# Optimization experiments

Hardware: AMD Instinct MI355X
Metric: run time of the kernel (lower is better)

Reference implementation:

```python
import jax, jax.numpy as jnp
from jax import lax
import numpy as np

N_BINS = 8
SIGMA = (1.0, 2.0)
ALPHA = (1.0, 2.0, 4.0)
BETA = (0.02, 0.05)
KSIZE = 7
BOUNDS = (0.0, 1.0)
C, H, W = 3, 512, 512


def gaussian_kernel(size, s):
    # matches torch: linspace(-size//2+1, size//2, size) == arange(size)-size//2 for odd size
    x = jnp.arange(size, dtype=jnp.float32) - size // 2
    g = jnp.exp(-(x[:, None] ** 2 + x[None, :] ** 2) / (2.0 * s ** 2))
    return g / jnp.sum(g)


def setup_inputs() -> dict:
    key = jax.random.key(0)
    im_th = jax.random.uniform(key, (H, W, C), dtype=jnp.float32)
    sks = max(3, int(SIGMA[-1] * 4))
    if sks % 2 == 0:
        sks += 1
    sigma_kernels = jnp.stack([gaussian_kernel(sks, s) for s in SIGMA])      # (S, Ks, Ks)
    alpha_kernels = jnp.stack([gaussian_kernel(KSIZE, a) for a in ALPHA])    # (A, k, k)
    edges = jnp.linspace(BOUNDS[0], BOUNDS[1], N_BINS + 1, dtype=jnp.float32)
    bin_centers = (edges[1:] + edges[:-1]) / 2.0                             # (N,)
    betas = jnp.array(BETA, dtype=jnp.float32)                               # (B,)
    return dict(im_th=im_th, sigma_kernels=sigma_kernels,
                alpha_kernels=alpha_kernels, bin_centers=bin_centers, betas=betas)


def _conv_per_channel(x, k):
    # x: (M, H, W); k: (K, kh, kw) -> (M, K, H, W). Channels treated as batch,
    # equivalent to torch grouped conv with groups=M and K kernels per group.
    p = k.shape[-1] // 2
    return lax.conv_general_dilated(x[:, None], k[:, None], (1, 1),
                                    [(p, p), (p, p)],
                                    dimension_numbers=('NCHW', 'OIHW', 'NCHW'))


def reference(im_th, sigma_kernels, alpha_kernels, bin_centers, betas):
    x = jnp.clip(im_th, 0.0, 1.0).transpose(2, 0, 1)  # (C, H, W)
    C_, H_, W_ = x.shape
    S = sigma_kernels.shape[0]
    A = alpha_kernels.shape[0]
    B = betas.shape[0]
    N = bin_centers.shape[0]
    # per-channel blur at each sigma: (C, S, H, W)
    conv = _conv_per_channel(x, sigma_kernels)
    # gaussian soft-binning: (B, N, C, S, H, W)
    diff = conv[None, None] - bin_centers[None, :, None, None, None, None]
    bv = betas[:, None, None, None, None, None]
    iso = jnp.exp(-0.5 * (diff / bv) ** 2) / (jnp.sqrt(2.0 * jnp.pi) * bv)
    # depthwise alpha aggregation over all B*N*C*S channels: (M, A, H, W)
    out = _conv_per_channel(iso.reshape(B * N * C_ * S, H_, W_), alpha_kernels)
    loi = out.reshape(B, N, C_, S, A, H_, W_).transpose(4, 0, 3, 2, 5, 6, 1)
    return loi  # (A, B, S, C, H, W, N)
```

## Files before the change

### kernel.cpp

```cpp
#include <hip/hip_runtime.h>
#include <hip/hip_fp16.h>

#define IMH 512
#define IMW 512


__device__ __forceinline__ __half2 bc_h2(int v) {
  union { int i; __half2 h; } u; u.i = v; return u.h;
}
__device__ __forceinline__ int bc_i(__half2 v) {
  union { int i; __half2 h; } u; u.h = v; return u.i;
}

__global__ __launch_bounds__(256, 6) void loi_fused(
    const float* __restrict__ im,
    const float* __restrict__ sigk,
    const float* __restrict__ alphak,
    const float* __restrict__ binc,
    const float* __restrict__ betas,
    float* __restrict__ out)
{
  const int t     = threadIdx.x;
  const int combo = blockIdx.z;
  const int b     = combo / 6;
  const int sc    = combo % 6;
  const int s     = sc / 3;
  const int c     = sc % 3;
  const int tx0   = blockIdx.x * 32;
  const int ty0   = blockIdx.y * 8;

  __shared__ __align__(16) float smt[560];
  __shared__ __align__(16) unsigned char uni[23104];
  __shared__ float kf[3][8];
  __shared__ float sf[12];

  float*  imt = (float*)uni;
  float*  svt = (float*)(uni + 4224);
  __half* iso = (__half*)uni;
  __half* vv  = (__half*)(uni + 8512);

  for (int e = t; e < 1056; e += 256) {
    int j = e / 48, i = e - j * 48;
    float v = 0.f;
    if (i < 46) {
      int gy = ty0 + j - 7, gx = tx0 + i - 7;
      if (gy >= 0 && gy < IMH && gx >= 0 && gx < IMW) {
        v = im[(gy * IMW + gx) * 3 + c];
        v = fminf(fmaxf(v, 0.f), 1.f);
      }
    }
    imt[e] = v;
  }
  if (t < 9) {
    float acc = 0.f;
    #pragma unroll
    for (int j = 0; j < 9; j++) acc += sigk[s * 81 + t * 9 + j];
    sf[t] = acc;
  }
  if (t >= 32 && t < 56) {
    int a = (t - 32) >> 3, d = t & 7;
    float v = 0.f;
    if (d < 7) {
      #pragma unroll
      for (int j = 0; j < 7; j++) v += alphak[a * 49 + d * 7 + j];
    }
    kf[a][d] = v;
  }
  __syncthreads();

  for (int e = t; e < 672; e += 256) {
    int rr = e / 48, i = e - rr * 48;
    if (i < 46) {
      float acc = 0.f;
      #pragma unroll
      for (int d = 0; d < 9; d++) acc = fmaf(sf[d], imt[(rr + d) * 48 + i], acc);
      svt[e] = acc;
    }
  }
  __syncthreads();

  for (int e = t; e < 560; e += 256) {
    int rr = e / 40, j = e - rr * 40;
    if (j < 38) {
      float acc = 0.f;
      #pragma unroll
      for (int d = 0; d < 9; d++) acc = fmaf(sf[d], svt[rr * 48 + j + d], acc);
      smt[e] = acc;
    }
  }
  __syncthreads();

  const float beta = betas[b];
  const float norm = 0.39894228040143268f / beta;
  const float c2   = -0.72134752044448170f / (beta * beta);
  const int   np   = t & 3;
  const float ctr0 = binc[2 * np];
  const float ctr1 = binc[2 * np + 1];
  for (int u = t; u < 2128; u += 256) {
    int q  = u >> 2;
    int rr = q / 38, jj = q - rr * 38;
    float v  = smt[rr * 40 + jj];
    float t0 = v - ctr0, t1 = v - ctr1;
    float E0 = exp2f(t0 * t0 * c2) * norm;
    float E1 = exp2f(t1 * t1 * c2) * norm;
    int X = tx0 + jj - 3, Y = ty0 + rr - 3;
    if (!(((unsigned)X < IMW) && ((unsigned)Y < IMH))) { E0 = 0.f; E1 = 0.f; }
    *(__half2*)(iso + q * 8 + np * 2) = __floats2half2_rn(E0, E1);
  }
  __syncthreads();

  __half2 kh[3][7];
  #pragma unroll
  for (int a = 0; a < 3; a++)
    #pragma unroll
    for (int d = 0; d < 7; d++) kh[a][d] = __float2half2_rn(kf[a][d]);

  for (int g = t; g < 304; g += 256) {
    int yr = g / 38, jj = g - yr * 38;
    const int base = yr * 38 + jj;
    __half2 acc[3][4];
    #pragma unroll
    for (int a = 0; a < 3; a++)
      #pragma unroll
      for (int q = 0; q < 4; q++) acc[a][q] = __floats2half2_rn(0.f, 0.f);
    #pragma unroll
    for (int d = 0; d < 7; d++) {
      int4 raw = *(const int4*)(iso + ((base + d * 38) << 3));
      __half2 w0 = bc_h2(raw.x), w1 = bc_h2(raw.y);
      __half2 w2 = bc_h2(raw.z), w3 = bc_h2(raw.w);
      #pragma unroll
      for (int a = 0; a < 3; a++) {
        acc[a][0] = __hfma2(kh[a][d], w0, acc[a][0]);
        acc[a][1] = __hfma2(kh[a][d], w1, acc[a][1]);
        acc[a][2] = __hfma2(kh[a][d], w2, acc[a][2]);
        acc[a][3] = __hfma2(kh[a][d], w3, acc[a][3]);
      }
    }
    #pragma unroll
    for (int a = 0; a < 3; a++) {
      int4 o;
      o.x = bc_i(acc[a][0]); o.y = bc_i(acc[a][1]);
      o.z = bc_i(acc[a][2]); o.w = bc_i(acc[a][3]);
      *(int4*)(vv + ((((a << 3) + yr) * 38 + jj) << 3)) = o;
    }
  }
  __syncthreads();

  const int col = t & 31;
  const int row = t >> 5;
  float* op = out + ((size_t)combo << 21)
                  + ((size_t)(ty0 + row) * 512 + (tx0 + col)) * 8;
  #pragma unroll
  for (int a = 0; a < 3; a++) {
    const int base = ((a << 3) + row) * 38 + col;
    __half2 pA0, pA1, pA2, pA3, pB0, pB1, pB2, pB3;
    {
      int4 r0 = *(const int4*)(vv + (base << 3));
      pA0 = __hmul2(kh[a][0], bc_h2(r0.x)); pA1 = __hmul2(kh[a][0], bc_h2(r0.y));
      pA2 = __hmul2(kh[a][0], bc_h2(r0.z)); pA3 = __hmul2(kh[a][0], bc_h2(r0.w));
      int4 r1 = *(const int4*)(vv + ((base + 1) << 3));
      pB0 = __hmul2(kh[a][1], bc_h2(r1.x)); pB1 = __hmul2(kh[a][1], bc_h2(r1.y));
      pB2 = __hmul2(kh[a][1], bc_h2(r1.z)); pB3 = __hmul2(kh[a][1], bc_h2(r1.w));
    }
    #pragma unroll
    for (int d = 2; d < 7; d += 2) {
      int4 rA = *(const int4*)(vv + ((base + d) << 3));
      pA0 = __hfma2(kh[a][d], bc_h2(rA.x), pA0);
      pA1 = __hfma2(kh[a][d], bc_h2(rA.y), pA1);
      pA2 = __hfma2(kh[a][d], bc_h2(rA.z), pA2);
      pA3 = __hfma2(kh[a][d], bc_h2(rA.w), pA3);
      if (d + 1 < 7) {
        int4 rB = *(const int4*)(vv + ((base + d + 1) << 3));
        pB0 = __hfma2(kh[a][d + 1], bc_h2(rB.x), pB0);
        pB1 = __hfma2(kh[a][d + 1], bc_h2(rB.y), pB1);
        pB2 = __hfma2(kh[a][d + 1], bc_h2(rB.z), pB2);
        pB3 = __hfma2(kh[a][d + 1], bc_h2(rB.w), pB3);
      }
    }
    float2 a0 = __half22float2(pA0), b0 = __half22float2(pB0);
    float2 a1 = __half22float2(pA1), b1 = __half22float2(pB1);
    float2 a2 = __half22float2(pA2), b2 = __half22float2(pB2);
    float2 a3 = __half22float2(pA3), b3 = __half22float2(pB3);
    float4 lo = make_float4(a0.x + b0.x, a0.y + b0.y, a1.x + b1.x, a1.y + b1.y);
    float4 hi = make_float4(a2.x + b2.x, a2.y + b2.y, a3.x + b3.x, a3.y + b3.y);
    float* p = op + ((size_t)(a * 12) << 21);
    *(float4*)p       = lo;
    *(float4*)(p + 4) = hi;
  }
}

extern "C" void kernel_launch(void* const* d_in, const int* in_sizes, int n_in,
                              void* d_out, int out_size, void* d_ws, size_t ws_size,
                              hipStream_t stream)
{
  const float* im   = (const float*)d_in[0];
  const float* sigk = (const float*)d_in[1];
  const float* alpk = (const float*)d_in[2];
  const float* binc = (const float*)d_in[3];
  const float* bets = (const float*)d_in[4];
  float* out = (float*)d_out;

  loi_fused<<<dim3(16, 64, 12), 256, 0, stream>>>(im, sigk, alpk, binc, bets, out);
}
```

Baseline: 324.8 us.

## Enlarge tile to 32x16 and fuse separable alpha pass into register accumulation

Doubles the output tile height to 16 rows, which shrinks halo overhead per output pixel. The two-pass half-precision alpha convolution is replaced by a single pass: each thread does the horizontal pass in fp16 and scatters results into fp32 register accumulators for four output rows. This removes the intermediate shared buffer and one barrier, and folds the normalization into the kernel weights. The sigma blur passes are vectorized with float4, and each thread now computes all eight bins. The vertical pass now accumulates in fp32, which changes precision slightly, and the extra accumulators raise register pressure.

```diff
diff --git a/kernel.cpp b/kernel.cpp
--- a/kernel.cpp
+++ b/kernel.cpp
@@ -3,6 +3,8 @@
 
 #define IMH 512
 #define IMW 512
+#define TW  32
+#define TH  16
 
 
 __device__ __forceinline__ __half2 bc_h2(int v) {
@@ -12,7 +14,7 @@
   union { int i; __half2 h; } u; u.h = v; return u.i;
 }
 
-__global__ __launch_bounds__(256, 6) void loi_fused(
+__global__ __launch_bounds__(256, 8) void loi_fused(
     const float* __restrict__ im,
     const float* __restrict__ sigk,
     const float* __restrict__ alphak,
@@ -26,25 +28,24 @@
   const int sc    = combo % 6;
   const int s     = sc / 3;
   const int c     = sc % 3;
-  const int tx0   = blockIdx.x * 32;
-  const int ty0   = blockIdx.y * 8;
-
-  __shared__ __align__(16) float smt[560];
-  __shared__ __align__(16) unsigned char uni[23104];
+  const int tx0   = blockIdx.x * TW;
+  const int ty0   = blockIdx.y * TH;
+
+  __shared__ __align__(16) float smt[22 * 40];
+  __shared__ __align__(16) unsigned char uni[13376];
   __shared__ float kf[3][8];
   __shared__ float sf[12];
 
   float*  imt = (float*)uni;
-  float*  svt = (float*)(uni + 4224);
+  float*  svt = (float*)(uni + 5760);
   __half* iso = (__half*)uni;
-  __half* vv  = (__half*)(uni + 8512);
-
-  for (int e = t; e < 1056; e += 256) {
+
+  for (int e = t; e < 1440; e += 256) {
     int j = e / 48, i = e - j * 48;
     float v = 0.f;
     if (i < 46) {
       int gy = ty0 + j - 7, gx = tx0 + i - 7;
-      if (gy >= 0 && gy < IMH && gx >= 0 && gx < IMW) {
+      if ((unsigned)gy < IMH && (unsigned)gx < IMW) {
         v = im[(gy * IMW + gx) * 3 + c];
         v = fminf(fmaxf(v, 0.f), 1.f);
       }
@@ -68,124 +69,135 @@
   }
   __syncthreads();
 
-  for (int e = t; e < 672; e += 256) {
-    int rr = e / 48, i = e - rr * 48;
-    if (i < 46) {
-      float acc = 0.f;
-      #pragma unroll
-      for (int d = 0; d < 9; d++) acc = fmaf(sf[d], imt[(rr + d) * 48 + i], acc);
-      svt[e] = acc;
-    }
-  }
-  __syncthreads();
-
-  for (int e = t; e < 560; e += 256) {
-    int rr = e / 40, j = e - rr * 40;
-    if (j < 38) {
-      float acc = 0.f;
-      #pragma unroll
-      for (int d = 0; d < 9; d++) acc = fmaf(sf[d], svt[rr * 48 + j + d], acc);
-      smt[e] = acc;
-    }
+  for (int u = t; u < 264; u += 256) {
+    int rr = u / 12, cu = u - rr * 12;
+    const float* p = imt + rr * 48 + cu * 4;
+    float4 acc = make_float4(0.f, 0.f, 0.f, 0.f);
+    #pragma unroll
+    for (int d = 0; d < 9; d++) {
+      float4 w = *(const float4*)(p + d * 48);
+      float sd = sf[d];
+      acc.x = fmaf(sd, w.x, acc.x); acc.y = fmaf(sd, w.y, acc.y);
+      acc.z = fmaf(sd, w.z, acc.z); acc.w = fmaf(sd, w.w, acc.w);
+    }
+    *(float4*)(svt + rr * 48 + cu * 4) = acc;
+  }
+  __syncthreads();
+
+  for (int u = t; u < 220; u += 256) {
+    int rr = u / 10, cu = u - rr * 10;
+    const float* p = svt + rr * 48 + cu * 4;
+    float v[16];
+    #pragma unroll
+    for (int q = 0; q < 4; q++) {
+      float4 w = *(const float4*)(p + q * 4);
+      v[4 * q + 0] = w.x; v[4 * q + 1] = w.y;
+      v[4 * q + 2] = w.z; v[4 * q + 3] = w.w;
+    }
+    float o0 = 0.f, o1 = 0.f, o2 = 0.f, o3 = 0.f;
+    #pragma unroll
+    for (int d = 0; d < 9; d++) {
+      float sd = sf[d];
+      o0 = fmaf(sd, v[d + 0], o0); o1 = fmaf(sd, v[d + 1], o1);
+      o2 = fmaf(sd, v[d + 2], o2); o3 = fmaf(sd, v[d + 3], o3);
+    }
+    *(float4*)(smt + rr * 40 + cu * 4) = make_float4(o0, o1, o2, o3);
   }
   __syncthreads();
 
   const float beta = betas[b];
+  const float c2   = -0.72134752044448170f / (beta * beta);
+  float bc0 = binc[0], bc1 = binc[1], bc2 = binc[2], bc3 = binc[3];
+  float bc4 = binc[4], bc5 = binc[5], bc6 = binc[6], bc7 = binc[7];
+  for (int p = t; p < 836; p += 256) {
+    int rr = p / 38, jj = p - rr * 38;
+    float v = smt[rr * 40 + jj];
+    int X = tx0 + jj - 3, Y = ty0 + rr - 3;
+    float msk = (((unsigned)X < IMW) && ((unsigned)Y < IMH)) ? 1.f : 0.f;
+    float t0 = v - bc0, t1 = v - bc1, t2 = v - bc2, t3 = v - bc3;
+    float t4 = v - bc4, t5 = v - bc5, t6 = v - bc6, t7 = v - bc7;
+    float E0 = exp2f(t0 * t0 * c2) * msk, E1 = exp2f(t1 * t1 * c2) * msk;
+    float E2 = exp2f(t2 * t2 * c2) * msk, E3 = exp2f(t3 * t3 * c2) * msk;
+    float E4 = exp2f(t4 * t4 * c2) * msk, E5 = exp2f(t5 * t5 * c2) * msk;
+    float E6 = exp2f(t6 * t6 * c2) * msk, E7 = exp2f(t7 * t7 * c2) * msk;
+    int4 w;
+    w.x = bc_i(__floats2half2_rn(E0, E1));
+    w.y = bc_i(__floats2half2_rn(E2, E3));
+    w.z = bc_i(__floats2half2_rn(E4, E5));
+    w.w = bc_i(__floats2half2_rn(E6, E7));
+    *(int4*)(iso + p * 8) = w;
+  }
+  __syncthreads();
+
   const float norm = 0.39894228040143268f / beta;
-  const float c2   = -0.72134752044448170f / (beta * beta);
-  const int   np   = t & 3;
-  const float ctr0 = binc[2 * np];
-  const float ctr1 = binc[2 * np + 1];
-  for (int u = t; u < 2128; u += 256) {
-    int q  = u >> 2;
-    int rr = q / 38, jj = q - rr * 38;
-    float v  = smt[rr * 40 + jj];
-    float t0 = v - ctr0, t1 = v - ctr1;
-    float E0 = exp2f(t0 * t0 * c2) * norm;
-    float E1 = exp2f(t1 * t1 * c2) * norm;
-    int X = tx0 + jj - 3, Y = ty0 + rr - 3;
-    if (!(((unsigned)X < IMW) && ((unsigned)Y < IMH))) { E0 = 0.f; E1 = 0.f; }
-    *(__half2*)(iso + q * 8 + np * 2) = __floats2half2_rn(E0, E1);
-  }
-  __syncthreads();
-
   __half2 kh[3][7];
+  float   kvf[3][7];
   #pragma unroll
   for (int a = 0; a < 3; a++)
     #pragma unroll
-    for (int d = 0; d < 7; d++) kh[a][d] = __float2half2_rn(kf[a][d]);
-
-  for (int g = t; g < 304; g += 256) {
-    int yr = g / 38, jj = g - yr * 38;
-    const int base = yr * 38 + jj;
-    __half2 acc[3][4];
-    #pragma unroll
-    for (int a = 0; a < 3; a++)
-      #pragma unroll
-      for (int q = 0; q < 4; q++) acc[a][q] = __floats2half2_rn(0.f, 0.f);
-    #pragma unroll
     for (int d = 0; d < 7; d++) {
-      int4 raw = *(const int4*)(iso + ((base + d * 38) << 3));
-      __half2 w0 = bc_h2(raw.x), w1 = bc_h2(raw.y);
-      __half2 w2 = bc_h2(raw.z), w3 = bc_h2(raw.w);
+      float f = kf[a][d];
+      kh[a][d]  = __float2half2_rn(f);
+      kvf[a][d] = f * norm;
+    }
+
+  const int ng  = t & 1;
+  const int col = (t >> 1) & 31;
+  const int rq  = t >> 6;
+  const int r0  = rq * 4;
+
+  float4 acc[4][3];
+  #pragma unroll
+  for (int j = 0; j < 4; j++)
+    #pragma unroll
+    for (int a = 0; a < 3; a++) acc[j][a] = make_float4(0.f, 0.f, 0.f, 0.f);
+
+  const __half* ibase = iso + ((r0 * 38 + col) * 8 + ng * 4);
+  #pragma unroll
+  for (int m = 0; m < 10; m++) {
+    const __half* prow = ibase + m * 304;
+    __half2 h0[3], h1[3];
+    #pragma unroll
+    for (int a = 0; a < 3; a++) {
+      h0[a] = __float2half2_rn(0.f);
+      h1[a] = __float2half2_rn(0.f);
+    }
+    #pragma unroll
+    for (int e = 0; e < 7; e++) {
+      int2 ve = *(const int2*)(prow + e * 8);
+      __half2 lo = bc_h2(ve.x), hi = bc_h2(ve.y);
       #pragma unroll
       for (int a = 0; a < 3; a++) {
-        acc[a][0] = __hfma2(kh[a][d], w0, acc[a][0]);
-        acc[a][1] = __hfma2(kh[a][d], w1, acc[a][1]);
-        acc[a][2] = __hfma2(kh[a][d], w2, acc[a][2]);
-        acc[a][3] = __hfma2(kh[a][d], w3, acc[a][3]);
+        h0[a] = __hfma2(kh[a][e], lo, h0[a]);
+        h1[a] = __hfma2(kh[a][e], hi, h1[a]);
       }
     }
     #pragma unroll
     for (int a = 0; a < 3; a++) {
-      int4 o;
-      o.x = bc_i(acc[a][0]); o.y = bc_i(acc[a][1]);
-      o.z = bc_i(acc[a][2]); o.w = bc_i(acc[a][3]);
-      *(int4*)(vv + ((((a << 3) + yr) * 38 + jj) << 3)) = o;
-    }
-  }
-  __syncthreads();
-
-  const int col = t & 31;
-  const int row = t >> 5;
-  float* op = out + ((size_t)combo << 21)
-                  + ((size_t)(ty0 + row) * 512 + (tx0 + col)) * 8;
-  #pragma unroll
-  for (int a = 0; a < 3; a++) {
-    const int base = ((a << 3) + row) * 38 + col;
-    __half2 pA0, pA1, pA2, pA3, pB0, pB1, pB2, pB3;
-    {
-      int4 r0 = *(const int4*)(vv + (base << 3));
-      pA0 = __hmul2(kh[a][0], bc_h2(r0.x)); pA1 = __hmul2(kh[a][0], bc_h2(r0.y));
-      pA2 = __hmul2(kh[a][0], bc_h2(r0.z)); pA3 = __hmul2(kh[a][0], bc_h2(r0.w));
-      int4 r1 = *(const int4*)(vv + ((base + 1) << 3));
-      pB0 = __hmul2(kh[a][1], bc_h2(r1.x)); pB1 = __hmul2(kh[a][1], bc_h2(r1.y));
-      pB2 = __hmul2(kh[a][1], bc_h2(r1.z)); pB3 = __hmul2(kh[a][1], bc_h2(r1.w));
-    }
-    #pragma unroll
-    for (int d = 2; d < 7; d += 2) {
-      int4 rA = *(const int4*)(vv + ((base + d) << 3));
-      pA0 = __hfma2(kh[a][d], bc_h2(rA.x), pA0);
-      pA1 = __hfma2(kh[a][d], bc_h2(rA.y), pA1);
-      pA2 = __hfma2(kh[a][d], bc_h2(rA.z), pA2);
-      pA3 = __hfma2(kh[a][d], bc_h2(rA.w), pA3);
-      if (d + 1 < 7) {
-        int4 rB = *(const int4*)(vv + ((base + d + 1) << 3));
-        pB0 = __hfma2(kh[a][d + 1], bc_h2(rB.x), pB0);
-        pB1 = __hfma2(kh[a][d + 1], bc_h2(rB.y), pB1);
-        pB2 = __hfma2(kh[a][d + 1], bc_h2(rB.z), pB2);
-        pB3 = __hfma2(kh[a][d + 1], bc_h2(rB.w), pB3);
+      float2 f0 = __half22float2(h0[a]);
+      float2 f1 = __half22float2(h1[a]);
+      #pragma unroll
+      for (int j = 0; j < 4; j++) {
+        if (m - j >= 0 && m - j <= 6) {
+          float w = kvf[a][m - j];
+          acc[j][a].x = fmaf(w, f0.x, acc[j][a].x);
+          acc[j][a].y = fmaf(w, f0.y, acc[j][a].y);
+          acc[j][a].z = fmaf(w, f1.x, acc[j][a].z);
+          acc[j][a].w = fmaf(w, f1.y, acc[j][a].w);
+        }
       }
     }
-    float2 a0 = __half22float2(pA0), b0 = __half22float2(pB0);
-    float2 a1 = __half22float2(pA1), b1 = __half22float2(pB1);
-    float2 a2 = __half22float2(pA2), b2 = __half22float2(pB2);
-    float2 a3 = __half22float2(pA3), b3 = __half22float2(pB3);
-    float4 lo = make_float4(a0.x + b0.x, a0.y + b0.y, a1.x + b1.x, a1.y + b1.y);
-    float4 hi = make_float4(a2.x + b2.x, a2.y + b2.y, a3.x + b3.x, a3.y + b3.y);
-    float* p = op + ((size_t)(a * 12) << 21);
-    *(float4*)p       = lo;
-    *(float4*)(p + 4) = hi;
+  }
+
+  const int gx = tx0 + col;
+  #pragma unroll
+  for (int j = 0; j < 4; j++) {
+    const int gy = ty0 + r0 + j;
+    float* op = out + ((size_t)combo << 21)
+                    + ((size_t)gy * 512 + gx) * 8 + ng * 4;
+    *(float4*)op                          = acc[j][0];
+    *(float4*)(op + ((size_t)12 << 21))   = acc[j][1];
+    *(float4*)(op + ((size_t)24 << 21))   = acc[j][2];
   }
 }
 
@@ -200,5 +212,6 @@
   const float* bets = (const float*)d_in[4];
   float* out = (float*)d_out;
 
-  loi_fused<<<dim3(16, 64, 12), 256, 0, stream>>>(im, sigk, alpk, binc, bets, out);
-}
+  loi_fused<<<dim3(512 / TW, 512 / TH, 12), 256, 0, stream>>>(
+      im, sigk, alpk, binc, bets, out);
+}
```

Result: slower. 1.171 ms (+260.5%).
